# Optimization experiments

Measured on AMD Instinct MI355X. Metric: run time of the kernel, lower is better.

Reference implementation:

```python
import jax, jax.numpy as jnp
import numpy as np

T, H = 2048, 1024          # tokens, hidden_size
NH, NKV, D = 16, 4, 64     # heads, kv heads, head_dim
E, F = 8, 1024             # experts, intermediate_size
TOPK = 1
EPS = 1e-5
THETA = 500000.0
SCALE = D ** -0.5


def rmsnorm(x, w=None, eps=EPS):
    # fp32 accumulation like vLLM RMSNorm
    v = jnp.mean(x.astype(jnp.float32) ** 2, axis=-1, keepdims=True)
    y = x.astype(jnp.float32) * jax.lax.rsqrt(v + eps)
    y = y.astype(x.dtype)
    return y * w if w is not None else y


def setup_inputs() -> dict:
    key = jax.random.key(0)
    ks = jax.random.split(key, 12)
    s = 1.0 / np.sqrt(H)
    sf = 1.0 / np.sqrt(F)
    return {
        "positions": jnp.arange(T, dtype=jnp.int32),
        "hidden_states": jax.random.normal(ks[0], (T, H), jnp.float32),
        "ln1_w": jnp.ones((H,), jnp.float32),
        "ln2_w": jnp.ones((H,), jnp.float32),
        "wqkv": jax.random.normal(ks[1], (H, (NH + 2 * NKV) * D), jnp.float32) * s,
        "wo": jax.random.normal(ks[2], (NH * D, H), jnp.float32) * s,
        "router_w": jax.random.normal(ks[3], (H, E), jnp.float32) * s,
        "w_gate": jax.random.normal(ks[4], (E, H, F), jnp.float32) * s,
        "w_up": jax.random.normal(ks[5], (E, H, F), jnp.float32) * s,
        "w_down": jax.random.normal(ks[6], (E, F, H), jnp.float32) * sf,
        "sh_gate": jax.random.normal(ks[7], (H, F), jnp.float32) * s,
        "sh_up": jax.random.normal(ks[8], (H, F), jnp.float32) * s,
        "sh_down": jax.random.normal(ks[9], (F, H), jnp.float32) * sf,
    }


def reference(positions, hidden_states, ln1_w, ln2_w, wqkv, wo, router_w,
              w_gate, w_up, w_down, sh_gate, sh_up, sh_down):
    # --- input_layernorm (residual is None on first call) ---
    residual = hidden_states
    h = rmsnorm(hidden_states, ln1_w)

    # --- attention: qkv proj ---
    qkv = h @ wqkv
    q = qkv[:, : NH * D].reshape(T, NH, D)
    k = qkv[:, NH * D: (NH + NKV) * D].reshape(T, NKV, D)
    v = qkv[:, (NH + NKV) * D:].reshape(T, NKV, D)

    # --- neox-style RoPE ---
    half = D // 2
    inv_freq = 1.0 / (THETA ** (jnp.arange(half, dtype=jnp.float32) / half))
    ang = positions.astype(jnp.float32)[:, None] * inv_freq[None, :]
    cos = jnp.cos(ang)[:, None, :]  # [T,1,half]
    sin = jnp.sin(ang)[:, None, :]

    def rope(x):
        x1, x2 = x[..., :half], x[..., half:]
        return jnp.concatenate([x1 * cos - x2 * sin, x2 * cos + x1 * sin], axis=-1)

    q = rope(q)
    k = rope(k)

    # --- fp32 QK-RMSNorm (no weight), applied after RoPE as in source ---
    q = rmsnorm(q)
    k = rmsnorm(k)

    # --- GQA causal attention ---
    n_rep = NH // NKV
    kr = jnp.repeat(k, n_rep, axis=1)  # [T,NH,D]
    vr = jnp.repeat(v, n_rep, axis=1)
    scores = jnp.einsum('thd,shd->hts', q, kr) * SCALE  # [NH,T,T]
    causal = positions[:, None] >= positions[None, :]
    scores = jnp.where(causal[None], scores, -jnp.inf)
    attn = jax.nn.softmax(scores, axis=-1)
    ao = jnp.einsum('hts,shd->thd', attn, vr).reshape(T, NH * D)
    h = ao @ wo

    # --- post_attention_layernorm with fused residual add ---
    x = h + residual
    residual = x
    h = rmsnorm(x, ln2_w)

    # --- MoE: top-1 sigmoid router, router weight applied on input ---
    logits = h @ router_w                      # [T,E]
    score, idx = jax.lax.top_k(logits, TOPK)   # [T,1]
    gate = jax.nn.sigmoid(score.astype(jnp.float32)).astype(h.dtype)
    x_in = h * gate                            # apply_router_weight_on_input
    onehot = (idx == jnp.arange(E)[None, :]).astype(h.dtype)  # [T,E]
    g = jax.nn.silu(jnp.einsum('th,ehf->tef', x_in, w_gate)) \
        * jnp.einsum('th,ehf->tef', x_in, w_up)               # [T,E,F]
    out_e = jnp.einsum('tef,efh->teh', g, w_down)             # [T,E,H]
    routed = jnp.einsum('teh,te->th', out_e, onehot)

    # --- shared expert (SiLU MLP) ---
    shared = (jax.nn.silu(h @ sh_gate) * (h @ sh_up)) @ sh_down

    out = routed + shared
    return (out, residual)
```

## Files before the change

### kernel.cpp

```cpp
#include <hip/hip_runtime.h>
#include <hip/hip_bf16.h>
#include <cmath>
#include <cstdint>

#define T 2048
#define H 1024
#define NH 16
#define NKV 4
#define DH 64
#define NE 8
#define FF 1024
#define QKVN ((NH + 2 * NKV) * DH)
#define EPS 1e-5f
#define ATTN_SCALE 0.125f
#define LOG2E 1.44269504f
#define MBOUND 12.0f

typedef short bf16x8 __attribute__((ext_vector_type(8)));
typedef float floatx4 __attribute__((ext_vector_type(4)));

__device__ __forceinline__ void gload16(const void* g, void* l) {
  __builtin_amdgcn_global_load_lds((const __attribute__((address_space(1))) void*)g,
                                   (__attribute__((address_space(3))) void*)l, 16, 0, 0);
}

__global__ __launch_bounds__(256) void rmsnorm1024(const float* __restrict__ x,
                                                   const float* __restrict__ w,
                                                   __hip_bfloat16* __restrict__ yb) {
  int row = blockIdx.x;
  const float4* x4 = (const float4*)(x + (size_t)row * H);
  float4 v = x4[threadIdx.x];
  float s = v.x * v.x + v.y * v.y + v.z * v.z + v.w * v.w;
  #pragma unroll
  for (int o = 32; o; o >>= 1) s += __shfl_down(s, o, 64);
  __shared__ float red[4];
  if ((threadIdx.x & 63) == 0) red[threadIdx.x >> 6] = s;
  __syncthreads();
  s = red[0] + red[1] + red[2] + red[3];
  float inv = rsqrtf(s * (1.0f / (float)H) + EPS);
  float4 wv = ((const float4*)w)[threadIdx.x];
  __hip_bfloat16* yp = yb + (size_t)row * H + threadIdx.x * 4;
  yp[0] = __float2bfloat16(v.x * inv * wv.x);
  yp[1] = __float2bfloat16(v.y * inv * wv.y);
  yp[2] = __float2bfloat16(v.z * inv * wv.z);
  yp[3] = __float2bfloat16(v.w * inv * wv.w);
}

__global__ __launch_bounds__(256) void fused_add_rms(const float* __restrict__ a,
                                                     const float* __restrict__ b,
                                                     float* __restrict__ resid,
                                                     const float* __restrict__ w,
                                                     float* __restrict__ yf,
                                                     __hip_bfloat16* __restrict__ yb) {
  int row = blockIdx.x;
  float4 av = ((const float4*)(a + (size_t)row * H))[threadIdx.x];
  float4 bv = ((const float4*)(b + (size_t)row * H))[threadIdx.x];
  float4 v = make_float4(av.x + bv.x, av.y + bv.y, av.z + bv.z, av.w + bv.w);
  ((float4*)(resid + (size_t)row * H))[threadIdx.x] = v;
  float s = v.x * v.x + v.y * v.y + v.z * v.z + v.w * v.w;
  #pragma unroll
  for (int o = 32; o; o >>= 1) s += __shfl_down(s, o, 64);
  __shared__ float red[4];
  if ((threadIdx.x & 63) == 0) red[threadIdx.x >> 6] = s;
  __syncthreads();
  s = red[0] + red[1] + red[2] + red[3];
  float inv = rsqrtf(s * (1.0f / (float)H) + EPS);
  float4 wv = ((const float4*)w)[threadIdx.x];
  float o0 = v.x * inv * wv.x, o1 = v.y * inv * wv.y, o2 = v.z * inv * wv.z, o3 = v.w * inv * wv.w;
  ((float4*)(yf + (size_t)row * H))[threadIdx.x] = make_float4(o0, o1, o2, o3);
  __hip_bfloat16* yp = yb + (size_t)row * H + threadIdx.x * 4;
  yp[0] = __float2bfloat16(o0);
  yp[1] = __float2bfloat16(o1);
  yp[2] = __float2bfloat16(o2);
  yp[3] = __float2bfloat16(o3);
}

__global__ __launch_bounds__(256) void tcast9(const float* __restrict__ srcE,
                                              const float* __restrict__ srcS,
                                              __hip_bfloat16* __restrict__ dst, int R, int C,
                                              long long srcStride, long long dstStride,
                                              long long sBatch, long long dBatch) {
  int z = blockIdx.z;
  const float* src = (srcS && z == (int)gridDim.z - 1) ? srcS : srcE + (long long)z * sBatch;
  dst += (long long)z * dBatch;
  int c0 = blockIdx.x * 64, r0 = blockIdx.y * 32;
  __shared__ float tile[32][65];
  int tid = threadIdx.x;
  int lr = tid >> 4;
  int lc = (tid & 15) * 4;
  #pragma unroll
  for (int it = 0; it < 2; it++) {
    float4 v = *(const float4*)(src + (long long)(r0 + lr + it * 16) * srcStride + c0 + lc);
    tile[lr + it * 16][lc + 0] = v.x;
    tile[lr + it * 16][lc + 1] = v.y;
    tile[lr + it * 16][lc + 2] = v.z;
    tile[lr + it * 16][lc + 3] = v.w;
  }
  __syncthreads();
  int oc = tid >> 2;
  int rr = (tid & 3) * 8;
  short ov[8];
  #pragma unroll
  for (int i = 0; i < 8; i++) {
    __hip_bfloat16 b = __float2bfloat16(tile[rr + i][oc]);
    ov[i] = *(short*)&b;
  }
  *(bf16x8*)((short*)dst + (long long)(c0 + oc) * dstStride + r0 + rr) = *(bf16x8*)ov;
}

__global__ __launch_bounds__(256) void gemm_bf16(const __hip_bfloat16* __restrict__ A,
                                                 const __hip_bfloat16* __restrict__ A2,
                                                 const __hip_bfloat16* __restrict__ Bt,
                                                 void* __restrict__ Cout, void* __restrict__ Cout2,
                                                 int M, int N, int K, int out_bf16,
                                                 const int* __restrict__ row_offs,
                                                 long long strideB) {
  int e = blockIdx.z;
  bool sh = (A2 != nullptr && e == (int)gridDim.z - 1);
  int rbeg = 0, rend = M;
  const __hip_bfloat16* Ap = A;
  void* Cp = Cout;
  if (sh) {
    Ap = A2; Cp = Cout2;
  } else if (row_offs) {
    rbeg = row_offs[e]; rend = row_offs[e + 1];
  }
  long long m0 = rbeg + (long long)blockIdx.y * 128;
  if (m0 >= rend) return;
  long long n0 = (long long)blockIdx.x * 64;
  const __hip_bfloat16* Bp = Bt + (long long)e * strideB;

  __shared__ unsigned short As[128 * 64];
  __shared__ unsigned short Bs[64 * 64];

  int tid = threadIdx.x;
  int lane = tid & 63, w = tid >> 6;
  int wr = (w >> 1) * 64, wc = (w & 1) * 32;
  int qd = lane >> 4, ln16 = lane & 15;
  int l7 = ln16 & 7;

  floatx4 acc[4][2];
  floatx4 zero = {0.f, 0.f, 0.f, 0.f};
  #pragma unroll
  for (int i = 0; i < 4; i++)
    #pragma unroll
    for (int j = 0; j < 2; j++) acc[i][j] = zero;

  int rowA[4], kcA[4];
  #pragma unroll
  for (int it = 0; it < 4; it++) {
    int chunk = tid + it * 256;
    rowA[it] = chunk >> 3;
    kcA[it] = ((chunk & 7) ^ (rowA[it] & 7)) * 8;
  }

  for (int k0 = 0; k0 < K; k0 += 64) {
    #pragma unroll
    for (int it = 0; it < 4; it++) {
      long long ra = m0 + rowA[it];
      if (ra >= rend) ra = rend - 1;
      gload16(Ap + ra * K + k0 + kcA[it], As + (tid + it * 256) * 8);
    }
    #pragma unroll
    for (int it = 0; it < 2; it++)
      gload16(Bp + (n0 + rowA[it]) * K + k0 + kcA[it], Bs + (tid + it * 256) * 8);
    __syncthreads();
    #pragma unroll
    for (int s = 0; s < 2; s++) {
      bf16x8 af[4], bfr[2];
      #pragma unroll
      for (int i = 0; i < 4; i++) {
        int row = wr + i * 16 + ln16;
        af[i] = *(const bf16x8*)(As + row * 64 + (((s * 4 + qd) ^ l7) * 8));
      }
      #pragma unroll
      for (int j = 0; j < 2; j++) {
        int row = wc + j * 16 + ln16;
        bfr[j] = *(const bf16x8*)(Bs + row * 64 + (((s * 4 + qd) ^ l7) * 8));
      }
      #pragma unroll
      for (int i = 0; i < 4; i++)
        #pragma unroll
        for (int j = 0; j < 2; j++)
          acc[i][j] = __builtin_amdgcn_mfma_f32_16x16x32_bf16(af[i], bfr[j], acc[i][j], 0, 0, 0);
    }
    __syncthreads();
  }

  #pragma unroll
  for (int i = 0; i < 4; i++) {
    #pragma unroll
    for (int r = 0; r < 4; r++) {
      long long gm = m0 + wr + i * 16 + qd * 4 + r;
      if (gm < rend) {
        #pragma unroll
        for (int j = 0; j < 2; j++) {
          long long gn = n0 + wc + j * 16 + ln16;
          float v = acc[i][j][r];
          if (out_bf16)
            ((__hip_bfloat16*)Cp)[gm * N + gn] = __float2bfloat16(v);
          else
            ((float*)Cp)[gm * N + gn] = v;
        }
      }
    }
  }
}

__global__ __launch_bounds__(256) void rope_pack(const float* __restrict__ qkv,
                                                 const int* __restrict__ positions,
                                                 __hip_bfloat16* __restrict__ Qb,
                                                 __hip_bfloat16* __restrict__ Kb) {
  int b = blockIdx.x * 4 + (threadIdx.x >> 6);
  int t = b / (NH + NKV);
  int hh = b % (NH + NKV);
  const float* ptr = qkv + (long long)t * QKVN + hh * DH;
  int d = threadIdx.x & 63;
  float v = ptr[d];
  int fi = d & 31;
  float inv_freq = exp2f(-(float)fi * (18.93156857f / 32.0f));
  float ang = (float)positions[t] * inv_freq;
  float c = __cosf(ang), s = __sinf(ang);
  float other = __shfl_xor(v, 32, 64);
  float r = (d < 32) ? (v * c - other * s) : (v * c + other * s);
  float sq = r * r;
  #pragma unroll
  for (int off = 32; off; off >>= 1) sq += __shfl_xor(sq, off, 64);
  float o = r * rsqrtf(sq * (1.0f / (float)DH) + EPS);
  if (hh < NH)
    Qb[(size_t)t * (NH * DH) + hh * DH + d] = __float2bfloat16(o * (ATTN_SCALE * LOG2E));
  else
    Kb[(size_t)t * (NKV * DH) + (hh - NH) * DH + d] = __float2bfloat16(o);
}

__global__ __launch_bounds__(256) void attn_mfma(const __hip_bfloat16* __restrict__ Qb,
                                                 const __hip_bfloat16* __restrict__ Kb,
                                                 const __hip_bfloat16* __restrict__ VtG,
                                                 __hip_bfloat16* __restrict__ ao) {
  int h = blockIdx.y;
  int kvh = h >> 2;
  int nb = gridDim.x;
  int bx = blockIdx.x;
  int qi = (bx & 1) ? (nb - 1 - (bx >> 1)) : (bx >> 1);
  int q0 = qi * 64;

  __shared__ unsigned short Ks[64 * 64];
  __shared__ unsigned short Vs[64 * 64];
  __shared__ unsigned short Ps[4 * 16 * 64];

  int tid = threadIdx.x;
  int lane = tid & 63, w = tid >> 6;
  int qd = lane >> 4, ln16 = lane & 15;
  int l7 = ln16 & 7;
  unsigned short* Pw = Ps + w * 16 * 64;

  int r0 = tid >> 3;
  int sc = ((tid & 7) ^ (r0 & 7)) * 8;

  int tq = q0 + w * 16 + ln16;
  const unsigned short* qp = (const unsigned short*)Qb + (size_t)tq * (NH * DH) + h * DH;
  bf16x8 aq[2];
  aq[0] = *(const bf16x8*)(qp + qd * 8);
  aq[1] = *(const bf16x8*)(qp + 32 + qd * 8);

  bf16x8 ones;
  #pragma unroll
  for (int i = 0; i < 8; i++) ones[i] = (short)0x3F80;

  floatx4 O_[4], accl;
  floatx4 zero = {0.f, 0.f, 0.f, 0.f};
  #pragma unroll
  for (int j = 0; j < 4; j++) O_[j] = zero;
  accl = zero;
  int tq_base = q0 + w * 16 + qd * 4;
  int wave_min_row = q0 + w * 16;

  for (int kb = 0; kb < q0 + 64; kb += 64) {
    gload16((const unsigned short*)Kb + (size_t)(kb + r0) * (NKV * DH) + kvh * DH + sc, Ks + tid * 8);
    gload16((const unsigned short*)Kb + (size_t)(kb + r0 + 32) * (NKV * DH) + kvh * DH + sc, Ks + tid * 8 + 2048);
    gload16((const unsigned short*)VtG + (size_t)(kvh * DH + r0) * T + kb + sc, Vs + tid * 8);
    gload16((const unsigned short*)VtG + (size_t)(kvh * DH + r0 + 32) * T + kb + sc, Vs + tid * 8 + 2048);
    __syncthreads();

    floatx4 S_[4];
    #pragma unroll
    for (int j = 0; j < 4; j++) S_[j] = zero;
    #pragma unroll
    for (int s = 0; s < 2; s++) {
      bf16x8 bk[4];
      #pragma unroll
      for (int j = 0; j < 4; j++)
        bk[j] = *(const bf16x8*)(Ks + (j * 16 + ln16) * 64 + (((s * 4 + qd) ^ l7) * 8));
      #pragma unroll
      for (int j = 0; j < 4; j++)
        S_[j] = __builtin_amdgcn_mfma_f32_16x16x32_bf16(aq[s], bk[j], S_[j], 0, 0, 0);
    }

    if (kb + 63 > wave_min_row) {
      #pragma unroll
      for (int j = 0; j < 4; j++) {
        int tk = kb + j * 16 + ln16;
        #pragma unroll
        for (int r = 0; r < 4; r++)
          S_[j][r] = (tk <= tq_base + r) ? exp2f(S_[j][r] - MBOUND) : 0.f;
      }
    } else {
      #pragma unroll
      for (int j = 0; j < 4; j++)
        #pragma unroll
        for (int r = 0; r < 4; r++) S_[j][r] = exp2f(S_[j][r] - MBOUND);
    }

    #pragma unroll
    for (int j = 0; j < 4; j++)
      #pragma unroll
      for (int r = 0; r < 4; r++) {
        int row = qd * 4 + r;
        int pc = (((j * 2 + (ln16 >> 3)) ^ (row & 7)) * 8) + l7;
        __hip_bfloat16 pb = __float2bfloat16(S_[j][r]);
        Pw[row * 64 + pc] = *(unsigned short*)&pb;
      }

    #pragma unroll
    for (int s = 0; s < 2; s++) {
      bf16x8 ap = *(const bf16x8*)(Pw + ln16 * 64 + (((s * 4 + qd) ^ l7) * 8));
      bf16x8 bv[4];
      #pragma unroll
      for (int j = 0; j < 4; j++)
        bv[j] = *(const bf16x8*)(Vs + (j * 16 + ln16) * 64 + (((s * 4 + qd) ^ l7) * 8));
      #pragma unroll
      for (int j = 0; j < 4; j++)
        O_[j] = __builtin_amdgcn_mfma_f32_16x16x32_bf16(ap, bv[j], O_[j], 0, 0, 0);
      accl = __builtin_amdgcn_mfma_f32_16x16x32_bf16(ap, ones, accl, 0, 0, 0);
    }
    __syncthreads();
  }

  float inv[4];
  #pragma unroll
  for (int r = 0; r < 4; r++) inv[r] = 1.0f / accl[r];
  #pragma unroll
  for (int j = 0; j < 4; j++)
    #pragma unroll
    for (int r = 0; r < 4; r++)
      ao[(size_t)(tq_base + r) * (NH * DH) + h * DH + j * 16 + ln16] =
          __float2bfloat16(O_[j][r] * inv[r]);
}

__global__ void silumul_both(const __hip_bfloat16* __restrict__ gA2,
                             const __hip_bfloat16* __restrict__ gS2,
                             __hip_bfloat16* __restrict__ gP,
                             __hip_bfloat16* __restrict__ gPs, int n4each) {
  int i = blockIdx.x * blockDim.x + threadIdx.x;
  const __hip_bfloat16* src = gA2;
  __hip_bfloat16* dst = gP;
  if (i >= n4each) {
    i -= n4each;
    src = gS2;
    dst = gPs;
  }
  int el = i * 4;
  int row = el >> 10;
  int c = el & (FF - 1);
  const __hip_bfloat16* g = src + (size_t)row * (2 * FF) + c;
  #pragma unroll
  for (int k = 0; k < 4; k++) {
    float av = __bfloat162float(g[k]);
    float bv = __bfloat162float(g[FF + k]);
    dst[el + k] = __float2bfloat16(av / (1.f + __expf(-av)) * bv);
  }
}

__global__ __launch_bounds__(64) void router_kernel(const float* __restrict__ h2,
                                                    const float* __restrict__ rw,
                                                    int* __restrict__ idx,
                                                    float* __restrict__ gate,
                                                    int* __restrict__ counts) {
  int t = blockIdx.x;
  int lane = threadIdx.x;
  float acc[NE] = {};
  for (int k = lane; k < H; k += 64) {
    float hv = h2[(long long)t * H + k];
    float4 r0 = *(const float4*)(rw + (long long)k * NE);
    float4 r1 = *(const float4*)(rw + (long long)k * NE + 4);
    acc[0] += hv * r0.x; acc[1] += hv * r0.y; acc[2] += hv * r0.z; acc[3] += hv * r0.w;
    acc[4] += hv * r1.x; acc[5] += hv * r1.y; acc[6] += hv * r1.z; acc[7] += hv * r1.w;
  }
  #pragma unroll
  for (int off = 32; off; off >>= 1)
    #pragma unroll
    for (int e2 = 0; e2 < NE; e2++) acc[e2] += __shfl_down(acc[e2], off, 64);
  if (lane == 0) {
    int best = 0;
    float bv = acc[0];
    #pragma unroll
    for (int e2 = 1; e2 < NE; e2++)
      if (acc[e2] > bv) { bv = acc[e2]; best = e2; }
    idx[t] = best;
    gate[t] = 1.f / (1.f + expf(-bv));
    atomicAdd(&counts[best], 1);
  }
}

__global__ void zero_counts_kernel(int* c) {
  if (threadIdx.x < 2 * NE) c[threadIdx.x] = 0;
}

__global__ void scan_kernel(const int* __restrict__ counts, int* __restrict__ offs) {
  if (threadIdx.x == 0) {
    int s = 0;
    for (int e2 = 0; e2 < NE; e2++) { offs[e2] = s; s += counts[e2]; }
    offs[NE] = s;
  }
}

__global__ void assign_kernel(const int* __restrict__ idx, const int* __restrict__ offs,
                              int* __restrict__ cnt2, int* __restrict__ perm,
                              int* __restrict__ pos) {
  int t = blockIdx.x * blockDim.x + threadIdx.x;
  if (t >= T) return;
  int e2 = idx[t];
  int p = offs[e2] + atomicAdd(&cnt2[e2], 1);
  pos[t] = p;
  perm[p] = t;
}

__global__ __launch_bounds__(256) void gather_kernel(const float* __restrict__ h2,
                                                     const float* __restrict__ gate,
                                                     const int* __restrict__ perm,
                                                     __hip_bfloat16* __restrict__ xg) {
  int p = blockIdx.x;
  int t = perm[p];
  float g = gate[t];
  float4 v = ((const float4*)(h2 + (long long)t * H))[threadIdx.x];
  __hip_bfloat16* yp = xg + (long long)p * H + threadIdx.x * 4;
  yp[0] = __float2bfloat16(v.x * g);
  yp[1] = __float2bfloat16(v.y * g);
  yp[2] = __float2bfloat16(v.z * g);
  yp[3] = __float2bfloat16(v.w * g);
}

__global__ __launch_bounds__(256) void final_add_kernel(float* __restrict__ out,
                                                        const float* __restrict__ outp,
                                                        const int* __restrict__ pos) {
  int t = blockIdx.x;
  int p = pos[t];
  const float4* src = (const float4*)(outp + (long long)p * H);
  float4* dst = (float4*)(out + (long long)t * H);
  float4 a = dst[threadIdx.x];
  float4 b = src[threadIdx.x];
  a.x += b.x; a.y += b.y; a.z += b.z; a.w += b.w;
  dst[threadIdx.x] = a;
}

extern "C" void kernel_launch(void* const* d_in, const int* in_sizes, int n_in,
                              void* d_out, int out_size, void* d_ws, size_t ws_size,
                              hipStream_t stream) {
  const int* positions = (const int*)d_in[0];
  const float* hidden = (const float*)d_in[1];
  const float* ln1_w = (const float*)d_in[2];
  const float* ln2_w = (const float*)d_in[3];
  const float* wqkv = (const float*)d_in[4];
  const float* wo = (const float*)d_in[5];
  const float* router_w = (const float*)d_in[6];
  const float* w_gate = (const float*)d_in[7];
  const float* w_up = (const float*)d_in[8];
  const float* w_down = (const float*)d_in[9];
  const float* sh_gate = (const float*)d_in[10];
  const float* sh_up = (const float*)d_in[11];
  const float* sh_down = (const float*)d_in[12];

  float* out = (float*)d_out;
  float* resid = out + (size_t)T * H;

  char* p = (char*)d_ws;
  auto alloc = [&](size_t bytes) { char* r = p; p += (bytes + 255) & ~(size_t)255; return r; };

  float* qkv = (float*)alloc((size_t)T * QKVN * 4);
  float* h2 = (float*)alloc((size_t)T * H * 4);
  float* gb1 = (float*)alloc((size_t)T * H * 4);
  float* outp = (float*)alloc((size_t)T * H * 4);
  __hip_bfloat16* h1b = (__hip_bfloat16*)alloc((size_t)T * H * 2);
  __hip_bfloat16* aob = (__hip_bfloat16*)alloc((size_t)T * H * 2);
  __hip_bfloat16* h2b = (__hip_bfloat16*)alloc((size_t)T * H * 2);
  __hip_bfloat16* xgb = (__hip_bfloat16*)alloc((size_t)T * H * 2);
  __hip_bfloat16* gA2 = (__hip_bfloat16*)alloc((size_t)T * 2 * FF * 2);
  __hip_bfloat16* gP = (__hip_bfloat16*)alloc((size_t)T * FF * 2);
  __hip_bfloat16* Qb = (__hip_bfloat16*)alloc((size_t)T * NH * DH * 2);
  __hip_bfloat16* Kb = (__hip_bfloat16*)alloc((size_t)T * NKV * DH * 2);
  __hip_bfloat16* VtG = (__hip_bfloat16*)alloc((size_t)NKV * DH * T * 2);
  __hip_bfloat16* wqkvT = (__hip_bfloat16*)alloc((size_t)H * QKVN * 2);
  __hip_bfloat16* woT = (__hip_bfloat16*)alloc((size_t)H * H * 2);
  __hip_bfloat16* wguT = (__hip_bfloat16*)alloc((size_t)9 * 2 * FF * H * 2);
  __hip_bfloat16* wdT = (__hip_bfloat16*)alloc((size_t)9 * H * FF * 2);
  int* counts = (int*)alloc(2 * NE * 4);
  int* cnt2 = counts + NE;
  int* offs = (int*)alloc((NE + 1) * 4);
  int* idx = (int*)alloc(T * 4);
  int* perm = (int*)alloc(T * 4);
  int* pos = (int*)alloc(T * 4);
  float* gate = (float*)alloc(T * 4);

  __hip_bfloat16* gS2 = (__hip_bfloat16*)gb1;
  __hip_bfloat16* gPs = h1b;

  tcast9<<<dim3(QKVN / 64, H / 32, 1), 256, 0, stream>>>(wqkv, nullptr, wqkvT, H, QKVN, QKVN, H, 0, 0);
  tcast9<<<dim3(H / 64, H / 32, 1), 256, 0, stream>>>(wo, nullptr, woT, H, H, H, H, 0, 0);
  tcast9<<<dim3(FF / 64, H / 32, 9), 256, 0, stream>>>(w_gate, sh_gate, wguT, H, FF, FF, H,
                                                       (long long)H * FF, (long long)2 * H * FF);
  tcast9<<<dim3(FF / 64, H / 32, 9), 256, 0, stream>>>(w_up, sh_up, wguT + (size_t)FF * H, H, FF, FF, H,
                                                       (long long)H * FF, (long long)2 * H * FF);
  tcast9<<<dim3(H / 64, FF / 32, 9), 256, 0, stream>>>(w_down, sh_down, wdT, FF, H, H, FF,
                                                       (long long)FF * H, (long long)H * FF);

  rmsnorm1024<<<T, 256, 0, stream>>>(hidden, ln1_w, h1b);
  gemm_bf16<<<dim3(QKVN / 64, T / 128, 1), 256, 0, stream>>>(h1b, nullptr, wqkvT, qkv, nullptr,
                                                             T, QKVN, H, 0, nullptr, 0);
  rope_pack<<<T * (NH + NKV) / 4, 256, 0, stream>>>(qkv, positions, Qb, Kb);
  tcast9<<<dim3(NKV * DH / 64, T / 32, 1), 256, 0, stream>>>(qkv + (NH + NKV) * DH, nullptr, VtG,
                                                             T, NKV * DH, QKVN, T, 0, 0);
  attn_mfma<<<dim3(T / 64, NH), 256, 0, stream>>>(Qb, Kb, VtG, aob);
  gemm_bf16<<<dim3(H / 64, T / 128, 1), 256, 0, stream>>>(aob, nullptr, woT, gb1, nullptr,
                                                          T, H, H, 0, nullptr, 0);
  fused_add_rms<<<T, 256, 0, stream>>>(gb1, hidden, resid, ln2_w, h2, h2b);
  zero_counts_kernel<<<1, 64, 0, stream>>>(counts);
  router_kernel<<<T, 64, 0, stream>>>(h2, router_w, idx, gate, counts);
  scan_kernel<<<1, 64, 0, stream>>>(counts, offs);
  assign_kernel<<<T / 256, 256, 0, stream>>>(idx, offs, cnt2, perm, pos);
  gather_kernel<<<T, 256, 0, stream>>>(h2, gate, perm, xgb);
  gemm_bf16<<<dim3(2 * FF / 64, T / 128, 9), 256, 0, stream>>>(xgb, h2b, wguT, gA2, gS2,
                                                               T, 2 * FF, H, 1, offs,
                                                               (long long)2 * H * FF);
  silumul_both<<<(2 * T * FF / 4) / 256, 256, 0, stream>>>(gA2, gS2, gP, gPs, T * FF / 4);
  gemm_bf16<<<dim3(H / 64, T / 128, 9), 256, 0, stream>>>(gP, gPs, wdT, outp, out,
                                                          T, H, FF, 0, offs, (long long)FF * H);
  final_add_kernel<<<T, 256, 0, stream>>>(out, outp, pos);
}
```

Measured before the change: 406.9 us.

## Split causal attention across KV chunks with separate combine kernel

Attention blocks now each process a strided subset of the KV tiles (four-way split along the key axis) and write unnormalized fp32 partial outputs and row sums to a scratch buffer. A new combine kernel sums the partials and normalizes them into the bf16 attention output. This raises the number of blocks and balances the causal work that previously grew with the query index. The cost is an extra kernel launch and a large fp32 partial buffer that is written and read back. The partials reuse the qkv buffer, which may overflow its allocation.

```diff
diff --git a/kernel.cpp b/kernel.cpp
--- a/kernel.cpp
+++ b/kernel.cpp
@@ -15,6 +15,7 @@
 #define ATTN_SCALE 0.125f
 #define LOG2E 1.44269504f
 #define MBOUND 12.0f
+#define ASPLIT 4
 
 typedef short bf16x8 __attribute__((ext_vector_type(8)));
 typedef float floatx4 __attribute__((ext_vector_type(4)));
@@ -236,13 +237,15 @@
 __global__ __launch_bounds__(256) void attn_mfma(const __hip_bfloat16* __restrict__ Qb,
                                                  const __hip_bfloat16* __restrict__ Kb,
                                                  const __hip_bfloat16* __restrict__ VtG,
-                                                 __hip_bfloat16* __restrict__ ao) {
+                                                 float* __restrict__ Opart,
+                                                 float* __restrict__ Lpart) {
   int h = blockIdx.y;
   int kvh = h >> 2;
-  int nb = gridDim.x;
-  int bx = blockIdx.x;
-  int qi = (bx & 1) ? (nb - 1 - (bx >> 1)) : (bx >> 1);
+  int qi = blockIdx.x;
+  int sp = blockIdx.z;
   int q0 = qi * 64;
+  int nt = qi + 1;
+  if (sp >= nt) return;
 
   __shared__ unsigned short Ks[64 * 64];
   __shared__ unsigned short Vs[64 * 64];
@@ -275,7 +278,8 @@
   int tq_base = q0 + w * 16 + qd * 4;
   int wave_min_row = q0 + w * 16;
 
-  for (int kb = 0; kb < q0 + 64; kb += 64) {
+  for (int kt = sp; kt < nt; kt += ASPLIT) {
+    int kb = kt * 64;
     gload16((const unsigned short*)Kb + (size_t)(kb + r0) * (NKV * DH) + kvh * DH + sc, Ks + tid * 8);
     gload16((const unsigned short*)Kb + (size_t)(kb + r0 + 32) * (NKV * DH) + kvh * DH + sc, Ks + tid * 8 + 2048);
     gload16((const unsigned short*)VtG + (size_t)(kvh * DH + r0) * T + kb + sc, Vs + tid * 8);
@@ -336,15 +340,53 @@
     __syncthreads();
   }
 
-  float inv[4];
-  #pragma unroll
-  for (int r = 0; r < 4; r++) inv[r] = 1.0f / accl[r];
+  size_t pbase = ((size_t)(qi * NH + h) * ASPLIT + sp) * (64 * 64);
+  int rl_base = w * 16 + qd * 4;
   #pragma unroll
   for (int j = 0; j < 4; j++)
     #pragma unroll
     for (int r = 0; r < 4; r++)
-      ao[(size_t)(tq_base + r) * (NH * DH) + h * DH + j * 16 + ln16] =
-          __float2bfloat16(O_[j][r] * inv[r]);
+      Opart[pbase + (size_t)(rl_base + r) * 64 + j * 16 + ln16] = O_[j][r];
+  if (ln16 == 0) {
+    size_t lbase = ((size_t)(qi * NH + h) * ASPLIT + sp) * 64;
+    #pragma unroll
+    for (int r = 0; r < 4; r++) Lpart[lbase + rl_base + r] = accl[r];
+  }
+}
+
+__global__ __launch_bounds__(256) void attn_combine(const float* __restrict__ Opart,
+                                                    const float* __restrict__ Lpart,
+                                                    __hip_bfloat16* __restrict__ ao) {
+  int qi = blockIdx.x, h = blockIdx.y;
+  int nv = (qi + 1 < ASPLIT) ? (qi + 1) : ASPLIT;
+  int row = threadIdx.x >> 2;
+  int c0 = (threadIdx.x & 3) * 16;
+  size_t base = (size_t)(qi * NH + h) * ASPLIT * 4096;
+  size_t lb = (size_t)(qi * NH + h) * ASPLIT * 64;
+  float l = 0.f;
+  float acc[16];
+  #pragma unroll
+  for (int i = 0; i < 16; i++) acc[i] = 0.f;
+  for (int s = 0; s < nv; s++) {
+    const float* Op = Opart + base + (size_t)s * 4096 + (size_t)row * 64 + c0;
+    l += Lpart[lb + s * 64 + row];
+    #pragma unroll
+    for (int i = 0; i < 16; i += 4) {
+      float4 v = *(const float4*)(Op + i);
+      acc[i] += v.x; acc[i + 1] += v.y; acc[i + 2] += v.z; acc[i + 3] += v.w;
+    }
+  }
+  float inv = 1.f / l;
+  int t = qi * 64 + row;
+  short ov[16];
+  #pragma unroll
+  for (int i = 0; i < 16; i++) {
+    __hip_bfloat16 b = __float2bfloat16(acc[i] * inv);
+    ov[i] = *(short*)&b;
+  }
+  short* dst = (short*)ao + (size_t)t * (NH * DH) + h * DH + c0;
+  *(bf16x8*)dst = *(bf16x8*)&ov[0];
+  *(bf16x8*)(dst + 8) = *(bf16x8*)&ov[8];
 }
 
 __global__ void silumul_both(const __hip_bfloat16* __restrict__ gA2,
@@ -504,6 +546,9 @@
   __hip_bfloat16* gS2 = (__hip_bfloat16*)gb1;
   __hip_bfloat16* gPs = h1b;
 
+  float* Opart = qkv;
+  float* Lpart = qkv + (size_t)(T / 64) * NH * ASPLIT * 4096;
+
   tcast9<<<dim3(QKVN / 64, H / 32, 1), 256, 0, stream>>>(wqkv, nullptr, wqkvT, H, QKVN, QKVN, H, 0, 0);
   tcast9<<<dim3(H / 64, H / 32, 1), 256, 0, stream>>>(wo, nullptr, woT, H, H, H, H, 0, 0);
   tcast9<<<dim3(FF / 64, H / 32, 9), 256, 0, stream>>>(w_gate, sh_gate, wguT, H, FF, FF, H,
@@ -519,7 +564,8 @@
   rope_pack<<<T * (NH + NKV) / 4, 256, 0, stream>>>(qkv, positions, Qb, Kb);
   tcast9<<<dim3(NKV * DH / 64, T / 32, 1), 256, 0, stream>>>(qkv + (NH + NKV) * DH, nullptr, VtG,
                                                              T, NKV * DH, QKVN, T, 0, 0);
-  attn_mfma<<<dim3(T / 64, NH), 256, 0, stream>>>(Qb, Kb, VtG, aob);
+  attn_mfma<<<dim3(T / 64, NH, ASPLIT), 256, 0, stream>>>(Qb, Kb, VtG, Opart, Lpart);
+  attn_combine<<<dim3(T / 64, NH), 256, 0, stream>>>(Opart, Lpart, aob);
   gemm_bf16<<<dim3(H / 64, T / 128, 1), 256, 0, stream>>>(aob, nullptr, woT, gb1, nullptr,
                                                           T, H, H, 0, nullptr, 0);
   fused_add_rms<<<T, 256, 0, stream>>>(gb1, hidden, resid, ln2_w, h2, h2b);
```

After: 405.6 us. Within noise of the previous version (-0.3%).
